# Kernel optimization log

Measured on AMD Instinct MI355X. Metric: run time of the kernel, lower is better.

## Reference

```python
import jax, jax.numpy as jnp
import numpy as np

EMBED, HEADS, LEVELS, POINTS = 256, 8, 4, 4
SPATIAL_SHAPES = np.array([[128, 128], [64, 64], [32, 32], [16, 16]], dtype=np.int32)


def _grid_init_bias():
    # Faithful reproduction of the sampling_offsets bias init (per-head directional grid).
    thetas = np.arange(HEADS, dtype=np.float32) * (2.0 * np.pi / HEADS)
    g = np.stack([np.cos(thetas), np.sin(thetas)], -1)
    g = g / np.abs(g).max(-1, keepdims=True)
    g = np.tile(g.reshape(HEADS, 1, 1, 2), (1, LEVELS, POINTS, 1))
    for i in range(POINTS):
        g[:, :, i, :] *= i + 1
    return g.reshape(-1).astype(np.float32)


def setup_inputs() -> dict:
    key = jax.random.key(0)
    ks = jax.random.split(key, 8)
    bs = 2
    V = int((SPATIAL_SHAPES[:, 0] * SPATIAL_SHAPES[:, 1]).sum())  # 21760
    Q = V  # encoder self-attention
    C = EMBED
    n_off = HEADS * LEVELS * POINTS * 2
    n_attn = HEADS * LEVELS * POINTS
    inv_sqrt_c = 1.0 / np.sqrt(C)
    return {
        "query": jax.random.normal(ks[0], (bs, Q, C), jnp.float32),
        "value": jax.random.normal(ks[1], (bs, V, C), jnp.float32),
        "reference_points": jax.random.uniform(ks[2], (bs, Q, LEVELS, 2), jnp.float32),
        "spatial_shapes": SPATIAL_SHAPES,  # static int array
        # learned parameters (torch Linear stored as [in, out]: y = x @ W + b)
        "W_off": jax.random.normal(ks[3], (C, n_off), jnp.float32) * 0.01,
        "b_off": jnp.asarray(_grid_init_bias()),
        "W_attn": jax.random.normal(ks[4], (C, n_attn), jnp.float32) * 0.02,
        "b_attn": jnp.zeros((n_attn,), jnp.float32),
        "W_v": jax.random.normal(ks[5], (C, C), jnp.float32) * inv_sqrt_c,
        "b_v": jnp.zeros((C,), jnp.float32),
        "W_out": jax.random.normal(ks[6], (C, C), jnp.float32) * inv_sqrt_c,
        "b_out": jnp.zeros((C,), jnp.float32),
    }


def _ms_deform_attn(query, value, reference_points, shapes,
                    W_off, b_off, W_attn, b_attn, W_v, b_v, W_out, b_out):
    bs, Q, C = query.shape
    d = C // HEADS
    # value projection -> [bs, heads, V, d]
    val = (value @ W_v + b_v).reshape(bs, -1, HEADS, d).transpose(0, 2, 1, 3)
    # sampling offsets and attention weights from query
    off = (query @ W_off + b_off).reshape(bs, Q, HEADS, LEVELS, POINTS, 2)
    attn = jax.nn.softmax(
        (query @ W_attn + b_attn).reshape(bs, Q, HEADS, LEVELS * POINTS), axis=-1
    ).reshape(bs, Q, HEADS, LEVELS, POINTS)
    # offset normalizer is (W, H) per level
    norm = jnp.asarray(np.stack([shapes[:, 1], shapes[:, 0]], -1), jnp.float32)  # [L,2]
    loc = reference_points[:, :, None, :, None, :] + off / norm[None, None, None, :, None, :]

    out = jnp.zeros((bs, HEADS, Q, d), query.dtype)
    start = 0
    for l in range(LEVELS):
        H, W = int(shapes[l, 0]), int(shapes[l, 1])
        v_l = val[:, :, start:start + H * W]  # [bs, heads, H*W, d]
        start += H * W
        loc_l = loc[:, :, :, l]    # [bs, Q, heads, P, 2] in [0,1]
        attn_l = attn[:, :, :, l]  # [bs, Q, heads, P]
        # grid_sample(align_corners=False, padding_mode='zeros') semantics
        g = 2.0 * loc_l - 1.0
        x = (g[..., 0] + 1.0) * 0.5 * W - 0.5
        y = (g[..., 1] + 1.0) * 0.5 * H - 0.5
        x0 = jnp.floor(x)
        y0 = jnp.floor(y)
        for dx in (0, 1):
            for dy in (0, 1):
                xi = x0 + dx
                yi = y0 + dy
                w = (1.0 - jnp.abs(x - xi)) * (1.0 - jnp.abs(y - yi))
                valid = (xi >= 0) & (xi <= W - 1) & (yi >= 0) & (yi <= H - 1)
                w = jnp.where(valid, w, 0.0) * attn_l  # fused corner + attention weight
                idx = (jnp.clip(yi, 0, H - 1).astype(jnp.int32) * W
                       + jnp.clip(xi, 0, W - 1).astype(jnp.int32))  # [bs,Q,heads,P]
                idx_t = jnp.transpose(idx, (0, 2, 1, 3)).reshape(bs, HEADS, Q * POINTS)
                vals = jnp.take_along_axis(v_l, idx_t[..., None], axis=2)
                vals = vals.reshape(bs, HEADS, Q, POINTS, d)
                out = out + jnp.einsum('bhqpd,bqhp->bhqd', vals, w)
    out = out.transpose(0, 2, 1, 3).reshape(bs, Q, C)  # heads-major channel layout
    return out @ W_out + b_out


def reference(query, value, reference_points, spatial_shapes,
              W_off, b_off, W_attn, b_attn, W_v, b_v, W_out, b_out):
    shapes = np.asarray(spatial_shapes)  # static
    return _ms_deform_attn(query, value, reference_points, shapes,
                           W_off, b_off, W_attn, b_attn, W_v, b_v, W_out, b_out)
```

## Files before the change

### kernel.cpp

```cpp
#include <hip/hip_runtime.h>
#include <math.h>

#define QN 21760
#define MTOT 43520
#define SZBQC 11141120

typedef __attribute__((ext_vector_type(8))) short bf16x8;
typedef __attribute__((ext_vector_type(4))) float f32x4;

__device__ inline ushort f2bf(float f) {
  union { float f; uint u; } v; v.f = f;
  return (ushort)((v.u + 0x7FFFu + ((v.u >> 16) & 1u)) >> 16);
}
__device__ inline uint pk2(float lo, float hi) { return (uint)f2bf(lo) | ((uint)f2bf(hi) << 16); }

__device__ inline void g2l(const ushort* g, ushort* l) {
  __builtin_amdgcn_global_load_lds(
      (const __attribute__((address_space(1))) void*)g,
      (__attribute__((address_space(3))) void*)l, 16, 0, 0);
}

__global__ __launch_bounds__(256) void prep_weights(
    const float* __restrict__ Wv, const float* __restrict__ Wout,
    const float* __restrict__ Woff, const float* __restrict__ Wattn,
    const float* __restrict__ boff, const float* __restrict__ battn,
    ushort* __restrict__ wv_t, ushort* __restrict__ wout_t,
    ushort* __restrict__ wol_t, float* __restrict__ biasf) {
  int bidx = blockIdx.x, t = threadIdx.x;
  if (bidx < 256) {
    int idx = bidx * 256 + t; int n = idx >> 8, k = idx & 255;
    wv_t[idx] = f2bf(Wv[(size_t)k * 256 + n]);
  } else if (bidx < 512) {
    int idx = (bidx - 256) * 256 + t; int n = idx >> 8, k = idx & 255;
    wout_t[idx] = f2bf(Wout[(size_t)k * 256 + n]);
  } else {
    int idx = (bidx - 512) * 256 + t; int n = idx >> 8, k = idx & 255;
    float v = (n < 256) ? Woff[(size_t)k * 256 + n] : Wattn[(size_t)k * 128 + (n - 256)];
    wol_t[idx] = f2bf(v);
    if (idx < 384) biasf[idx] = (idx < 256) ? boff[idx] : battn[idx - 256];
  }
}


__global__ __launch_bounds__(256) void gemm_in(
    const float* __restrict__ value, const float* __restrict__ query,
    const ushort* __restrict__ Wv, const ushort* __restrict__ Wol,
    const float* __restrict__ bv, const float* __restrict__ bol,
    ushort* __restrict__ val_out, float* __restrict__ offlog, int bx0) {
  __shared__ ushort As[2][4096];
  __shared__ ushort Bs[2][4096];
  const int t = threadIdx.x, wave = t >> 6, lane = t & 63;
  const int bx = bx0 + blockIdx.y, bm = blockIdx.x * 128;
  const bool isVal = bx < 2;
  const float* A   = isVal ? value : query;
  const ushort* Bt = isVal ? (Wv + (size_t)bx * 128 * 256)
                           : (Wol + (size_t)(bx - 2) * 128 * 256);
  const int wm = (wave >> 1) * 64, wn = (wave & 1) * 64;
  const int l15 = lane & 15, l4 = lane >> 4;
  const int pc = l4 ^ ((l15 >> 1) & 3);

  const int srow = lane >> 2;
  const int sch  = (lane & 3) ^ ((lane >> 3) & 3);
  const ushort* Bg = Bt + (size_t)(32 * wave + srow) * 256 + sch * 8;
  ushort* lb[2] = { &Bs[0][(32 * wave) * 32], &Bs[1][(32 * wave) * 32] };

  f32x4 acc[4][4];
#pragma unroll
  for (int i = 0; i < 4; ++i)
#pragma unroll
    for (int j = 0; j < 4; ++j) acc[i][j] = (f32x4){0.f, 0.f, 0.f, 0.f};

  int arow[4], apart[4];
#pragma unroll
  for (int i = 0; i < 4; ++i) {
    int c = t + i * 256; arow[i] = c >> 3; apart[i] = c & 7;
  }

  {
    float4 pa[4];
#pragma unroll
    for (int i = 0; i < 4; ++i)
      pa[i] = *(const float4*)&A[(size_t)(bm + arow[i]) * 256 + apart[i] * 4];
    g2l(Bg, lb[0]); g2l(Bg + 16 * 256, lb[0] + 16 * 32);
#pragma unroll
    for (int i = 0; i < 4; ++i) {
      int pc16 = (apart[i] >> 1) ^ ((arow[i] >> 1) & 3);
      ushort4 hv = { f2bf(pa[i].x), f2bf(pa[i].y), f2bf(pa[i].z), f2bf(pa[i].w) };
      *(ushort4*)&As[0][arow[i] * 32 + pc16 * 8 + (apart[i] & 1) * 4] = hv;
    }
  }

  for (int k = 0; k < 8; ++k) {
    __syncthreads();
    const int cur = k & 1, nxt = cur ^ 1;
    float4 pa[4];
    if (k < 7) {
      int k1 = (k + 1) * 32;
#pragma unroll
      for (int i = 0; i < 4; ++i)
        pa[i] = *(const float4*)&A[(size_t)(bm + arow[i]) * 256 + k1 + apart[i] * 4];
      g2l(Bg + k1, lb[nxt]); g2l(Bg + 16 * 256 + k1, lb[nxt] + 16 * 32);
    }
    bf16x8 af[4], bfr[4];
#pragma unroll
    for (int mi = 0; mi < 4; ++mi)
      af[mi] = *(const bf16x8*)&As[cur][(wm + mi * 16 + l15) * 32 + pc * 8];
#pragma unroll
    for (int ni = 0; ni < 4; ++ni)
      bfr[ni] = *(const bf16x8*)&Bs[cur][(wn + ni * 16 + l15) * 32 + pc * 8];
#pragma unroll
    for (int mi = 0; mi < 4; ++mi)
#pragma unroll
      for (int ni = 0; ni < 4; ++ni)
        acc[mi][ni] = __builtin_amdgcn_mfma_f32_16x16x32_bf16(af[mi], bfr[ni], acc[mi][ni], 0, 0, 0);
    if (k < 7) {
#pragma unroll
      for (int i = 0; i < 4; ++i) {
        int pc16 = (apart[i] >> 1) ^ ((arow[i] >> 1) & 3);
        ushort4 hv = { f2bf(pa[i].x), f2bf(pa[i].y), f2bf(pa[i].z), f2bf(pa[i].w) };
        *(ushort4*)&As[nxt][arow[i] * 32 + pc16 * 8 + (apart[i] & 1) * 4] = hv;
      }
    }
  }

  if (isVal) {
    _Float16* vo = (_Float16*)val_out;
#pragma unroll
    for (int mi = 0; mi < 4; ++mi)
#pragma unroll
      for (int ni = 0; ni < 4; ++ni) {
        int col = bx * 128 + wn + ni * 16 + l15;
        float bb = bv[col];
        int hh = col >> 5, c = col & 31;
#pragma unroll
        for (int r = 0; r < 4; ++r) {
          int row = bm + wm + mi * 16 + l4 * 4 + r;
          int b = (row >= QN) ? 1 : 0;
          int vpos = row - b * QN;
          vo[((size_t)(b * 8 + hh) * QN + vpos) * 32 + c] = (_Float16)(acc[mi][ni][r] + bb);
        }
      }
  } else {
#pragma unroll
    for (int mi = 0; mi < 4; ++mi)
#pragma unroll
      for (int ni = 0; ni < 4; ++ni) {
        int col = (bx - 2) * 128 + wn + ni * 16 + l15;
        float bb = bol[col];
#pragma unroll
        for (int r = 0; r < 4; ++r) {
          int row = bm + wm + mi * 16 + l4 * 4 + r;
          offlog[(size_t)row * 384 + col] = acc[mi][ni][r] + bb;
        }
      }
  }
}

__global__ __launch_bounds__(256) void gemm_out(
    const ushort* __restrict__ A, const ushort* __restrict__ Bt,
    const float* __restrict__ bias, float* __restrict__ C) {
  __shared__ ushort As[2][4096];
  __shared__ ushort Bs[2][4096];
  const int t = threadIdx.x, wave = t >> 6, lane = t & 63;
  const int bm = blockIdx.x * 128, bn = blockIdx.y * 128;
  const int wm = (wave >> 1) * 64, wn = (wave & 1) * 64;
  const int l15 = lane & 15, l4 = lane >> 4;
  const int pc = l4 ^ ((l15 >> 1) & 3);

  const int srow = lane >> 2;
  const int sch  = (lane & 3) ^ ((lane >> 3) & 3);
  const ushort* Ag = A + (size_t)(bm + 32 * wave + srow) * 256 + sch * 8;
  const ushort* Bg = Bt + (size_t)(bn + 32 * wave + srow) * 256 + sch * 8;
  ushort* la[2] = { &As[0][(32 * wave) * 32], &As[1][(32 * wave) * 32] };
  ushort* lb[2] = { &Bs[0][(32 * wave) * 32], &Bs[1][(32 * wave) * 32] };

  f32x4 acc[4][4];
#pragma unroll
  for (int i = 0; i < 4; ++i)
#pragma unroll
    for (int j = 0; j < 4; ++j) acc[i][j] = (f32x4){0.f, 0.f, 0.f, 0.f};

  g2l(Ag, la[0]); g2l(Ag + 16 * 256, la[0] + 16 * 32);
  g2l(Bg, lb[0]); g2l(Bg + 16 * 256, lb[0] + 16 * 32);

  for (int k = 0; k < 8; ++k) {
    __syncthreads();
    const int cur = k & 1, nxt = cur ^ 1;
    if (k < 7) {
      int k1 = (k + 1) * 32;
      g2l(Ag + k1, la[nxt]); g2l(Ag + 16 * 256 + k1, la[nxt] + 16 * 32);
      g2l(Bg + k1, lb[nxt]); g2l(Bg + 16 * 256 + k1, lb[nxt] + 16 * 32);
    }
    bf16x8 af[4], bfr[4];
#pragma unroll
    for (int mi = 0; mi < 4; ++mi)
      af[mi] = *(const bf16x8*)&As[cur][(wm + mi * 16 + l15) * 32 + pc * 8];
#pragma unroll
    for (int ni = 0; ni < 4; ++ni)
      bfr[ni] = *(const bf16x8*)&Bs[cur][(wn + ni * 16 + l15) * 32 + pc * 8];
#pragma unroll
    for (int mi = 0; mi < 4; ++mi)
#pragma unroll
      for (int ni = 0; ni < 4; ++ni)
        acc[mi][ni] = __builtin_amdgcn_mfma_f32_16x16x32_bf16(af[mi], bfr[ni], acc[mi][ni], 0, 0, 0);
  }

#pragma unroll
  for (int mi = 0; mi < 4; ++mi)
#pragma unroll
    for (int ni = 0; ni < 4; ++ni) {
      int col = bn + wn + ni * 16 + l15;
      float bb = bias[col];
#pragma unroll
      for (int r = 0; r < 4; ++r) {
        int row = bm + wm + mi * 16 + l4 * 4 + r;
        C[(size_t)row * 256 + col] = acc[mi][ni][r] + bb;
      }
    }
}

__device__ inline void fmah(float* a, uint4 u, float wv) {
  union { uint4 u; _Float16 h[8]; } c; c.u = u;
#pragma unroll
  for (int i = 0; i < 8; ++i) a[i] = fmaf((float)c.h[i], wv, a[i]);
}

__global__ __launch_bounds__(256) void msda_sample(
    const ushort* __restrict__ val, const float* __restrict__ offlog,
    const float* __restrict__ ref, ushort* __restrict__ interm, int vb0) {
  int vb  = vb0 + blockIdx.x;
  int h   = vb & 7;
  int z   = vb >> 3;
  int s   = threadIdx.x & 7;
  int o   = s & 3;
  int pp  = s >> 2;
  bool xs = s >= 4;
  int bq  = z * 32 + (threadIdx.x >> 3);
  int b   = (bq >= QN) ? 1 : 0;
  const ushort* vbl = val + (size_t)((uint)(b * 8 + h) * (uint)QN) * 32u + (uint)(s * 8);

  const float* lgp = offlog + (size_t)bq * 384 + 256 + h * 16;
  float2 lg = *(const float2*)(lgp + o * 4 + pp * 2);
  float m = fmaxf(lg.x, lg.y);
  m = fmaxf(m, __shfl_xor(m, 1, 64));
  m = fmaxf(m, __shfl_xor(m, 2, 64));
  m = fmaxf(m, __shfl_xor(m, 4, 64));
  float e0 = __expf(lg.x - m), e1 = __expf(lg.y - m);
  float ssum = e0 + e1;
  ssum += __shfl_xor(ssum, 1, 64);
  ssum += __shfl_xor(ssum, 2, 64);
  ssum += __shfl_xor(ssum, 4, 64);
  float inv = __builtin_amdgcn_rcpf(ssum);
  float aw0 = e0 * inv, aw1 = e1 * inv;

  const int  Wl  = 128 >> o;
  const uint t16 = 65536u >> (o + o);
  const int  lst = (int)((65536u - t16) / 3u);
  const float fW = (float)Wl;
  const float* offp = offlog + (size_t)bq * 384 + h * 32;
  float4 f0 = *(const float4*)(offp + o * 8 + pp * 4);
  float2 rf = *(const float2*)(ref + (size_t)bq * 8 + o * 2);
  const float xb = rf.x * fW - 0.5f;
  const float yb = rf.y * fW - 0.5f;
  float ox[2] = { f0.x, f0.z };
  float oy[2] = { f0.y, f0.w };
  float awq[2] = { aw0, aw1 };

  uint  pA0[2], pA1[2];
  float pW0[2], pW1[2], pY0[2], pY1[2];
#pragma unroll
  for (int q = 0; q < 2; ++q) {
    float x = xb + ox[q], y = yb + oy[q];
    float x0f = floorf(x), y0f = floorf(y);
    float fx = x - x0f, fy = y - y0f;
    int x0 = (int)x0f, y0 = (int)y0f;
    float a = awq[q];
    float wx0 = ((uint)x0       < (uint)Wl) ? (1.f - fx) : 0.f;
    float wx1 = ((uint)(x0 + 1) < (uint)Wl) ? fx         : 0.f;
    pY0[q] = (((uint)y0       < (uint)Wl) ? (1.f - fy) : 0.f) * a;
    pY1[q] = (((uint)(y0 + 1) < (uint)Wl) ? fy         : 0.f) * a;
    int xc0 = min(max(x0, 0), Wl - 1);
    int xc1 = min(max(x0 + 1, 0), Wl - 1);
    int yc0 = min(max(y0, 0), Wl - 1);
    int yc1 = min(max(y0 + 1, 0), Wl - 1);
    int xbase = min(max(x0, 0), Wl - 2);
    pW0[q] = ((xbase     == xc0) ? wx0 : 0.f) + ((xbase     == xc1) ? wx1 : 0.f);
    pW1[q] = ((xbase + 1 == xc0) ? wx0 : 0.f) + ((xbase + 1 == xc1) ? wx1 : 0.f);
    pA0[q] = (uint)((lst + yc0 * Wl + xbase) * 32);
    pA1[q] = (uint)((lst + yc1 * Wl + xbase) * 32);
  }

  float acc[8];
#pragma unroll
  for (int i = 0; i < 8; ++i) acc[i] = 0.f;

  const int gb = (threadIdx.x & 63) & ~7;

  uint  bA0[2], bA1[2];
  float bW[2], bY0[2], bY1[2];
  uint4 u0[2], u1[2];

#define MSDA_BCAST(J, S) do {                                   \
    const int l_ = (J) >> 2, p_ = (J) & 3;                      \
    const int src_ = gb | ((p_ >> 1) << 2) | l_;                \
    const int q_ = p_ & 1;                                      \
    bA0[S] = (uint)__shfl((int)pA0[q_], src_, 64);              \
    bA1[S] = (uint)__shfl((int)pA1[q_], src_, 64);              \
    float w0_ = __shfl(pW0[q_], src_, 64);                      \
    float w1_ = __shfl(pW1[q_], src_, 64);                      \
    bW[S]  = xs ? w1_ : w0_;                                    \
    bY0[S] = __shfl(pY0[q_], src_, 64);                         \
    bY1[S] = __shfl(pY1[q_], src_, 64);                         \
  } while (0)
#define MSDA_LOAD(S) do {                                       \
    u0[S] = *(const uint4*)(vbl + bA0[S]);                      \
    u1[S] = *(const uint4*)(vbl + bA1[S]);                      \
  } while (0)

  MSDA_BCAST(0, 0);
  MSDA_LOAD(0);
#pragma unroll
  for (int j = 0; j < 16; ++j) {
    const int cur = j & 1, nxt = cur ^ 1;
    if (j < 15) { MSDA_BCAST(j + 1, nxt); MSDA_LOAD(nxt); }
    fmah(acc, u0[cur], bW[cur] * bY0[cur]);
    fmah(acc, u1[cur], bW[cur] * bY1[cur]);
  }
#undef MSDA_BCAST
#undef MSDA_LOAD

#pragma unroll
  for (int i = 0; i < 8; ++i) acc[i] += __shfl_xor(acc[i], 4, 64);

  uint2 ov;
  if (!xs) { ov.x = pk2(acc[0], acc[1]); ov.y = pk2(acc[2], acc[3]); }
  else     { ov.x = pk2(acc[4], acc[5]); ov.y = pk2(acc[6], acc[7]); }
  *(uint2*)(interm + (size_t)bq * 256 + h * 32 + (s & 3) * 8 + (xs ? 4 : 0)) = ov;
}

extern "C" void kernel_launch(void* const* d_in, const int* in_sizes, int n_in,
                              void* d_out, int out_size, void* d_ws, size_t ws_size,
                              hipStream_t stream) {
  const float* query = (const float*)d_in[0];
  const float* value = (const float*)d_in[1];
  const float* ref   = (const float*)d_in[2];
  const float* W_off  = (const float*)d_in[4];
  const float* b_off  = (const float*)d_in[5];
  const float* W_attn = (const float*)d_in[6];
  const float* b_attn = (const float*)d_in[7];
  const float* W_v    = (const float*)d_in[8];
  const float* b_v    = (const float*)d_in[9];
  const float* W_out  = (const float*)d_in[10];
  const float* b_out  = (const float*)d_in[11];
  float* out = (float*)d_out;

  char* wsb = (char*)d_ws;
  ushort* ws_wv     = (ushort*)(wsb + 0);
  ushort* ws_wol    = (ushort*)(wsb + 131072);
  ushort* ws_wout   = (ushort*)(wsb + 327680);
  float*  ws_biasf  = (float*)(wsb + 458752);
  ushort* ws_val    = (ushort*)(wsb + 462848);
  ushort* ws_interm = (ushort*)(wsb + 22745088);
  float*  ws_offlog = (float*)(wsb + 45027328);
  size_t need = (size_t)45027328 + 66846720;
  if (ws_size < need) return;

  dim3 blk(256);
  prep_weights<<<dim3(896), blk, 0, stream>>>(W_v, W_out, W_off, W_attn, b_off, b_attn,
                                              ws_wv, ws_wout, ws_wol, ws_biasf);
  gemm_in<<<dim3(340, 2), blk, 0, stream>>>(value, query, ws_wv, ws_wol, b_v, ws_biasf,
                                            ws_val, ws_offlog, 0);
  gemm_in<<<dim3(340, 3), blk, 0, stream>>>(value, query, ws_wv, ws_wol, b_v, ws_biasf,
                                            ws_val, ws_offlog, 2);
  msda_sample<<<dim3(2720), blk, 0, stream>>>(ws_val, ws_offlog, ref, ws_interm, 0);
  msda_sample<<<dim3(2720), blk, 0, stream>>>(ws_val, ws_offlog, ref, ws_interm, 2720);
  msda_sample<<<dim3(2720), blk, 0, stream>>>(ws_val, ws_offlog, ref, ws_interm, 5440);
  msda_sample<<<dim3(2720), blk, 0, stream>>>(ws_val, ws_offlog, ref, ws_interm, 8160);
  gemm_out<<<dim3(340, 2), blk, 0, stream>>>(ws_interm, ws_wout, b_out, out);
}
```

Baseline: 286.6 us.

## Triple-buffer LDS in input/output GEMMs with prefetch distance two

Both projection GEMMs now use three LDS stages instead of two and issue global-to-LDS loads two k-steps ahead. __syncthreads is replaced by explicit vmcnt/lgkmcnt waits plus s_barrier, and the A-side fp32 register prefetch ping-pongs between two register sets. The aim is to hide global load latency behind MFMA work. The cost is 50% more LDS per block, which may reduce occupancy, and more registers.

```diff
diff --git a/kernel.cpp b/kernel.cpp
--- a/kernel.cpp
+++ b/kernel.cpp
@@ -47,8 +47,8 @@
     const ushort* __restrict__ Wv, const ushort* __restrict__ Wol,
     const float* __restrict__ bv, const float* __restrict__ bol,
     ushort* __restrict__ val_out, float* __restrict__ offlog, int bx0) {
-  __shared__ ushort As[2][4096];
-  __shared__ ushort Bs[2][4096];
+  __shared__ ushort As[3][4096];
+  __shared__ ushort Bs[3][4096];
   const int t = threadIdx.x, wave = t >> 6, lane = t & 63;
   const int bx = bx0 + blockIdx.y, bm = blockIdx.x * 128;
   const bool isVal = bx < 2;
@@ -62,7 +62,8 @@
   const int srow = lane >> 2;
   const int sch  = (lane & 3) ^ ((lane >> 3) & 3);
   const ushort* Bg = Bt + (size_t)(32 * wave + srow) * 256 + sch * 8;
-  ushort* lb[2] = { &Bs[0][(32 * wave) * 32], &Bs[1][(32 * wave) * 32] };
+  ushort* lb[3] = { &Bs[0][(32 * wave) * 32], &Bs[1][(32 * wave) * 32],
+                    &Bs[2][(32 * wave) * 32] };
 
   f32x4 acc[4][4];
 #pragma unroll
@@ -76,52 +77,68 @@
     int c = t + i * 256; arow[i] = c >> 3; apart[i] = c & 7;
   }
 
-  {
-    float4 pa[4];
-#pragma unroll
-    for (int i = 0; i < 4; ++i)
-      pa[i] = *(const float4*)&A[(size_t)(bm + arow[i]) * 256 + apart[i] * 4];
-    g2l(Bg, lb[0]); g2l(Bg + 16 * 256, lb[0] + 16 * 32);
-#pragma unroll
-    for (int i = 0; i < 4; ++i) {
-      int pc16 = (apart[i] >> 1) ^ ((arow[i] >> 1) & 3);
-      ushort4 hv = { f2bf(pa[i].x), f2bf(pa[i].y), f2bf(pa[i].z), f2bf(pa[i].w) };
-      *(ushort4*)&As[0][arow[i] * 32 + pc16 * 8 + (apart[i] & 1) * 4] = hv;
-    }
-  }
-
+#define GIN_LOADA(dst, koff) do {                                          \
+    _Pragma("unroll")                                                      \
+    for (int i_ = 0; i_ < 4; ++i_)                                         \
+      dst[i_] = *(const float4*)&A[(size_t)(bm + arow[i_]) * 256 + (koff) + apart[i_] * 4]; \
+  } while (0)
+#define GIN_STOREA(buf, src) do {                                          \
+    _Pragma("unroll")                                                      \
+    for (int i_ = 0; i_ < 4; ++i_) {                                       \
+      int pc16_ = (apart[i_] >> 1) ^ ((arow[i_] >> 1) & 3);                \
+      ushort4 hv_ = { f2bf(src[i_].x), f2bf(src[i_].y),                    \
+                      f2bf(src[i_].z), f2bf(src[i_].w) };                  \
+      *(ushort4*)&As[buf][arow[i_] * 32 + pc16_ * 8 + (apart[i_] & 1) * 4] = hv_; \
+    }                                                                      \
+  } while (0)
+
+  float4 paA[4], paB[4];
+  g2l(Bg, lb[0]);       g2l(Bg + 16 * 256, lb[0] + 16 * 32);
+  g2l(Bg + 32, lb[1]);  g2l(Bg + 16 * 256 + 32, lb[1] + 16 * 32);
+  GIN_LOADA(paA, 0);
+  GIN_LOADA(paB, 32);
+  GIN_STOREA(0, paA);
+  asm volatile("s_waitcnt lgkmcnt(0)" ::: "memory");
+
+#pragma unroll
   for (int k = 0; k < 8; ++k) {
-    __syncthreads();
-    const int cur = k & 1, nxt = cur ^ 1;
-    float4 pa[4];
-    if (k < 7) {
-      int k1 = (k + 1) * 32;
-#pragma unroll
-      for (int i = 0; i < 4; ++i)
-        pa[i] = *(const float4*)&A[(size_t)(bm + arow[i]) * 256 + k1 + apart[i] * 4];
-      g2l(Bg + k1, lb[nxt]); g2l(Bg + 16 * 256 + k1, lb[nxt] + 16 * 32);
+    const int cb = k % 3;
+    const int sb = (k + 2) % 3;
+    if (k < 7) { asm volatile("s_waitcnt vmcnt(6)" ::: "memory"); }
+    else       { asm volatile("s_waitcnt vmcnt(0)" ::: "memory"); }
+    __builtin_amdgcn_sched_barrier(0);
+    __builtin_amdgcn_s_barrier();
+    __builtin_amdgcn_sched_barrier(0);
+    if (k + 2 <= 7) {
+      int k2 = (k + 2) * 32;
+      g2l(Bg + k2, lb[sb]); g2l(Bg + 16 * 256 + k2, lb[sb] + 16 * 32);
     }
     bf16x8 af[4], bfr[4];
 #pragma unroll
     for (int mi = 0; mi < 4; ++mi)
-      af[mi] = *(const bf16x8*)&As[cur][(wm + mi * 16 + l15) * 32 + pc * 8];
+      af[mi] = *(const bf16x8*)&As[cb][(wm + mi * 16 + l15) * 32 + pc * 8];
 #pragma unroll
     for (int ni = 0; ni < 4; ++ni)
-      bfr[ni] = *(const bf16x8*)&Bs[cur][(wn + ni * 16 + l15) * 32 + pc * 8];
+      bfr[ni] = *(const bf16x8*)&Bs[cb][(wn + ni * 16 + l15) * 32 + pc * 8];
 #pragma unroll
     for (int mi = 0; mi < 4; ++mi)
 #pragma unroll
       for (int ni = 0; ni < 4; ++ni)
         acc[mi][ni] = __builtin_amdgcn_mfma_f32_16x16x32_bf16(af[mi], bfr[ni], acc[mi][ni], 0, 0, 0);
     if (k < 7) {
-#pragma unroll
-      for (int i = 0; i < 4; ++i) {
-        int pc16 = (apart[i] >> 1) ^ ((arow[i] >> 1) & 3);
-        ushort4 hv = { f2bf(pa[i].x), f2bf(pa[i].y), f2bf(pa[i].z), f2bf(pa[i].w) };
-        *(ushort4*)&As[nxt][arow[i] * 32 + pc16 * 8 + (apart[i] & 1) * 4] = hv;
+      const int wbuf = (k + 1) % 3;
+      if ((k & 1) == 0) {
+        GIN_STOREA(wbuf, paB);
+        if (k + 2 <= 7) GIN_LOADA(paA, (k + 2) * 32);
+      } else {
+        GIN_STOREA(wbuf, paA);
+        if (k + 2 <= 7) GIN_LOADA(paB, (k + 2) * 32);
       }
     }
-  }
+    asm volatile("s_waitcnt lgkmcnt(0)" ::: "memory");
+  }
+#undef GIN_LOADA
+#undef GIN_STOREA
 
   if (isVal) {
     _Float16* vo = (_Float16*)val_out;
@@ -159,8 +176,8 @@
 __global__ __launch_bounds__(256) void gemm_out(
     const ushort* __restrict__ A, const ushort* __restrict__ Bt,
     const float* __restrict__ bias, float* __restrict__ C) {
-  __shared__ ushort As[2][4096];
-  __shared__ ushort Bs[2][4096];
+  __shared__ ushort As[3][4096];
+  __shared__ ushort Bs[3][4096];
   const int t = threadIdx.x, wave = t >> 6, lane = t & 63;
   const int bm = blockIdx.x * 128, bn = blockIdx.y * 128;
   const int wm = (wave >> 1) * 64, wn = (wave & 1) * 64;
@@ -171,8 +188,10 @@
   const int sch  = (lane & 3) ^ ((lane >> 3) & 3);
   const ushort* Ag = A + (size_t)(bm + 32 * wave + srow) * 256 + sch * 8;
   const ushort* Bg = Bt + (size_t)(bn + 32 * wave + srow) * 256 + sch * 8;
-  ushort* la[2] = { &As[0][(32 * wave) * 32], &As[1][(32 * wave) * 32] };
-  ushort* lb[2] = { &Bs[0][(32 * wave) * 32], &Bs[1][(32 * wave) * 32] };
+  ushort* la[3] = { &As[0][(32 * wave) * 32], &As[1][(32 * wave) * 32],
+                    &As[2][(32 * wave) * 32] };
+  ushort* lb[3] = { &Bs[0][(32 * wave) * 32], &Bs[1][(32 * wave) * 32],
+                    &Bs[2][(32 * wave) * 32] };
 
   f32x4 acc[4][4];
 #pragma unroll
@@ -180,24 +199,32 @@
 #pragma unroll
     for (int j = 0; j < 4; ++j) acc[i][j] = (f32x4){0.f, 0.f, 0.f, 0.f};
 
-  g2l(Ag, la[0]); g2l(Ag + 16 * 256, la[0] + 16 * 32);
-  g2l(Bg, lb[0]); g2l(Bg + 16 * 256, lb[0] + 16 * 32);
-
+  g2l(Ag, la[0]);      g2l(Ag + 16 * 256, la[0] + 16 * 32);
+  g2l(Bg, lb[0]);      g2l(Bg + 16 * 256, lb[0] + 16 * 32);
+  g2l(Ag + 32, la[1]); g2l(Ag + 16 * 256 + 32, la[1] + 16 * 32);
+  g2l(Bg + 32, lb[1]); g2l(Bg + 16 * 256 + 32, lb[1] + 16 * 32);
+
+#pragma unroll
   for (int k = 0; k < 8; ++k) {
-    __syncthreads();
-    const int cur = k & 1, nxt = cur ^ 1;
-    if (k < 7) {
-      int k1 = (k + 1) * 32;
-      g2l(Ag + k1, la[nxt]); g2l(Ag + 16 * 256 + k1, la[nxt] + 16 * 32);
-      g2l(Bg + k1, lb[nxt]); g2l(Bg + 16 * 256 + k1, lb[nxt] + 16 * 32);
+    const int cb = k % 3;
+    const int sb = (k + 2) % 3;
+    if (k < 7) { asm volatile("s_waitcnt vmcnt(4)" ::: "memory"); }
+    else       { asm volatile("s_waitcnt vmcnt(0)" ::: "memory"); }
+    __builtin_amdgcn_sched_barrier(0);
+    __builtin_amdgcn_s_barrier();
+    __builtin_amdgcn_sched_barrier(0);
+    if (k + 2 <= 7) {
+      int k2 = (k + 2) * 32;
+      g2l(Ag + k2, la[sb]); g2l(Ag + 16 * 256 + k2, la[sb] + 16 * 32);
+      g2l(Bg + k2, lb[sb]); g2l(Bg + 16 * 256 + k2, lb[sb] + 16 * 32);
     }
     bf16x8 af[4], bfr[4];
 #pragma unroll
     for (int mi = 0; mi < 4; ++mi)
-      af[mi] = *(const bf16x8*)&As[cur][(wm + mi * 16 + l15) * 32 + pc * 8];
+      af[mi] = *(const bf16x8*)&As[cb][(wm + mi * 16 + l15) * 32 + pc * 8];
 #pragma unroll
     for (int ni = 0; ni < 4; ++ni)
-      bfr[ni] = *(const bf16x8*)&Bs[cur][(wn + ni * 16 + l15) * 32 + pc * 8];
+      bfr[ni] = *(const bf16x8*)&Bs[cb][(wn + ni * 16 + l15) * 32 + pc * 8];
 #pragma unroll
     for (int mi = 0; mi < 4; ++mi)
 #pragma unroll
```

Result: no change. 281.3 us (-1.8%).
